# Kernel tuning notes

Measured on AMD Instinct MI355X. Metric: run time of the kernel, lower is better.

Reference implementation:

```python
import jax, jax.numpy as jnp
import numpy as np

IDENT_SIZE = 100000
E = 1024      # embedding_dim == lstm input size
H = 2048      # hidden_dim
R = 1024      # remainder_dim
RULES = 50000 # rules_size


def setup_inputs() -> dict:
    key = jax.random.key(0)
    ks = jax.random.split(key, 12)
    def w(k, shape, scale=0.02):
        return jax.random.normal(k, shape, dtype=jnp.float32) * scale
    return {
        "ident": jax.random.randint(ks[0], (1,), 0, IDENT_SIZE),
        "remainder": jax.random.normal(ks[1], (1, 1, R), dtype=jnp.float32),
        "h0": jax.random.normal(ks[2], (1, 1, H), dtype=jnp.float32),
        "c0": jax.random.normal(ks[3], (1, 1, H), dtype=jnp.float32),
        "emb": w(ks[4], (IDENT_SIZE, E)),
        "W_rin": w(ks[5], (R, E)),   # linear_remainder_in, stored [in, out]
        "b_rin": jnp.zeros((E,), jnp.float32),
        "W_ih": w(ks[6], (4 * H, E)),  # torch LSTM weight_ih_l0, gate order i,f,g,o
        "W_hh": w(ks[7], (4 * H, H)),  # torch LSTM weight_hh_l0
        "b_ih": jnp.zeros((4 * H,), jnp.float32),
        "b_hh": jnp.zeros((4 * H,), jnp.float32),
        "W_ro": w(ks[8], (H, R)),      # linear_remainder_out
        "b_ro": jnp.zeros((R,), jnp.float32),
        "W_out": w(ks[9], (H, RULES)),  # linear_out
        "b_out": jnp.zeros((RULES,), jnp.float32),
    }


def reference(ident, remainder, h0, c0, emb, W_rin, b_rin, W_ih, W_hh,
              b_ih, b_hh, W_ro, b_ro, W_out, b_out):
    # embeds = embedding(ident).view((1,-1))  -> [1, E]
    embeds = emb[ident].reshape(1, -1)
    # inputs = embeds + relu(linear_remainder_in(remainder)) -> broadcast [1,1,E]
    x = embeds + jax.nn.relu(remainder @ W_rin + b_rin)  # [1,1,E]
    # single-step LSTM (seq=1, batch=1), torch gate order i, f, g, o
    gates = x @ W_ih.T + b_ih + h0 @ W_hh.T + b_hh  # [1,1,4H]
    i, f, g, o = jnp.split(gates, 4, axis=-1)
    c = jax.nn.sigmoid(f) * c0 + jax.nn.sigmoid(i) * jnp.tanh(g)
    h = jax.nn.sigmoid(o) * jnp.tanh(c)  # lstm_out == h for seq=1
    remainder_out = jax.nn.relu(h @ W_ro + b_ro)             # [1,1,R]
    out = jax.nn.log_softmax(jax.nn.relu(h @ W_out + b_out), axis=2)  # [1,1,RULES]
    return (out, (h, c), remainder_out)
```

## Files before the change

### kernel.cpp

```cpp
#include <hip/hip_runtime.h>
#include <math.h>

#define E_DIM 1024
#define H_DIM 2048
#define R_DIM 1024
#define RULES 50000

#define OUT_H  50000
#define OUT_C  52048
#define OUT_RO 54096

#define WS_XP    0
#define WS_H     8192
#define WS_PL    10240
#define WS_LOG   810240
#define WS_BSUM  860240
#define WS_PRO   860292

__device__ __forceinline__ float sigf(float x) { return 1.f / (1.f + expf(-x)); }

__global__ __launch_bounds__(256) void k_x_partial(const float* __restrict__ rem,
    const float* __restrict__ W_rin, float* __restrict__ xp)
{
    __shared__ float rs[128];
    int ec = blockIdx.x, rc = blockIdx.y;
    if (threadIdx.x < 128) rs[threadIdx.x] = rem[rc * 128 + threadIdx.x];
    __syncthreads();
    int e = ec * 256 + threadIdx.x;
    const float* base = W_rin + (size_t)rc * 128 * E_DIM + e;
    float acc = 0.f;
#pragma unroll 8
    for (int rr = 0; rr < 128; ++rr)
        acc = fmaf(rs[rr], base[(size_t)rr * E_DIM], acc);
    xp[rc * E_DIM + e] = acc;
}

__global__ __launch_bounds__(256) void k_lstm(const float* __restrict__ xp,
    const float* __restrict__ b_rin, const float* __restrict__ emb,
    const int* __restrict__ ident,
    const float* __restrict__ h0, const float* __restrict__ c0,
    const float* __restrict__ W_ih, const float* __restrict__ W_hh,
    const float* __restrict__ b_ih, const float* __restrict__ b_hh,
    float* __restrict__ d_out, float* __restrict__ ws_h)
{
    __shared__ float xs[E_DIM];
    long long row = (long long)ident[0] * E_DIM;
#pragma unroll
    for (int e = threadIdx.x; e < E_DIM; e += 256) {
        float s = 0.f;
#pragma unroll
        for (int rc = 0; rc < 8; ++rc) s += xp[rc * E_DIM + e];
        xs[e] = emb[row + e] + fmaxf(s + b_rin[e], 0.f);
    }
    __syncthreads();

    int k = blockIdx.x;
    int w = threadIdx.x >> 6, lane = threadIdx.x & 63;
    int j = w * H_DIM + k;
    const float4* Wi = (const float4*)(W_ih + (size_t)j * E_DIM);
    const float4* Wh = (const float4*)(W_hh + (size_t)j * H_DIM);
    const float4* x4 = (const float4*)xs;
    const float4* h4 = (const float4*)h0;
    float acc = 0.f;
#pragma unroll
    for (int s = 0; s < 4; ++s) {
        int idx = s * 64 + lane;
        float4 wv = Wi[idx], xv = x4[idx];
        acc += wv.x * xv.x + wv.y * xv.y + wv.z * xv.z + wv.w * xv.w;
    }
#pragma unroll
    for (int s = 0; s < 8; ++s) {
        int idx = s * 64 + lane;
        float4 wv = Wh[idx], hv = h4[idx];
        acc += wv.x * hv.x + wv.y * hv.y + wv.z * hv.z + wv.w * hv.w;
    }
#pragma unroll
    for (int off = 32; off > 0; off >>= 1) acc += __shfl_xor(acc, off);
    __shared__ float gl[4];
    if (lane == 0) gl[w] = acc + b_ih[j] + b_hh[j];
    __syncthreads();
    if (threadIdx.x == 0) {
        float gi = gl[0], gf = gl[1], gg = gl[2], go = gl[3];
        float c = sigf(gf) * c0[k] + sigf(gi) * tanhf(gg);
        float h = sigf(go) * tanhf(c);
        d_out[OUT_H + k] = h;
        d_out[OUT_C + k] = c;
        ws_h[k] = h;
    }
}

__global__ __launch_bounds__(256) void k_big_partial(const float* __restrict__ h,
    const float* __restrict__ W_out, const float* __restrict__ W_ro,
    float* __restrict__ pl, float* __restrict__ pro)
{
    __shared__ float hs[128];
    int hc = blockIdx.y;
    if (threadIdx.x < 128) hs[threadIdx.x] = h[hc * 128 + threadIdx.x];
    __syncthreads();
    if (blockIdx.x < 49) {
        int j0 = blockIdx.x * 1024 + threadIdx.x * 4;
        if (j0 >= RULES) return;
        float4 acc = {0.f, 0.f, 0.f, 0.f};
        const float* base = W_out + (size_t)hc * 128 * RULES + j0;
#pragma unroll 8
        for (int hh = 0; hh < 128; ++hh) {
            float hv = hs[hh];
            float4 wv = *(const float4*)(base + (size_t)hh * RULES);
            acc.x = fmaf(hv, wv.x, acc.x);
            acc.y = fmaf(hv, wv.y, acc.y);
            acc.z = fmaf(hv, wv.z, acc.z);
            acc.w = fmaf(hv, wv.w, acc.w);
        }
        *(float4*)(pl + (size_t)hc * RULES + j0) = acc;
    } else {
        int j0 = threadIdx.x * 4;
        float4 acc = {0.f, 0.f, 0.f, 0.f};
        const float* base = W_ro + (size_t)hc * 128 * R_DIM + j0;
#pragma unroll 8
        for (int hh = 0; hh < 128; ++hh) {
            float hv = hs[hh];
            float4 wv = *(const float4*)(base + (size_t)hh * R_DIM);
            acc.x = fmaf(hv, wv.x, acc.x);
            acc.y = fmaf(hv, wv.y, acc.y);
            acc.z = fmaf(hv, wv.z, acc.z);
            acc.w = fmaf(hv, wv.w, acc.w);
        }
        *(float4*)(pro + hc * R_DIM + j0) = acc;
    }
}

__global__ __launch_bounds__(256) void k_final(const float* __restrict__ pl,
    const float* __restrict__ b_out, const float* __restrict__ pro,
    const float* __restrict__ b_ro, float* __restrict__ logits,
    float* __restrict__ bsum, float* __restrict__ out_ro)
{
    if (blockIdx.x < 49) {
        int j0 = blockIdx.x * 1024 + threadIdx.x * 4;
        float se = 0.f;
        if (j0 < RULES) {
            float4 s = {0.f, 0.f, 0.f, 0.f};
#pragma unroll
            for (int hc = 0; hc < 16; ++hc) {
                float4 p = *(const float4*)(pl + (size_t)hc * RULES + j0);
                s.x += p.x; s.y += p.y; s.z += p.z; s.w += p.w;
            }
            float4 b = *(const float4*)(b_out + j0);
            float4 l;
            l.x = fmaxf(s.x + b.x, 0.f);
            l.y = fmaxf(s.y + b.y, 0.f);
            l.z = fmaxf(s.z + b.z, 0.f);
            l.w = fmaxf(s.w + b.w, 0.f);
            *(float4*)(logits + j0) = l;
            se = expf(l.x) + expf(l.y) + expf(l.z) + expf(l.w);
        }
        __shared__ float red[256];
        red[threadIdx.x] = se;
        __syncthreads();
        for (int off = 128; off > 0; off >>= 1) {
            if (threadIdx.x < off) red[threadIdx.x] += red[threadIdx.x + off];
            __syncthreads();
        }
        if (threadIdx.x == 0) bsum[blockIdx.x] = red[0];
    } else {
        int j0 = threadIdx.x * 4;
        float4 s = {0.f, 0.f, 0.f, 0.f};
#pragma unroll
        for (int hc = 0; hc < 16; ++hc) {
            float4 p = *(const float4*)(pro + hc * R_DIM + j0);
            s.x += p.x; s.y += p.y; s.z += p.z; s.w += p.w;
        }
        float4 b = *(const float4*)(b_ro + j0);
        float4 o;
        o.x = fmaxf(s.x + b.x, 0.f);
        o.y = fmaxf(s.y + b.y, 0.f);
        o.z = fmaxf(s.z + b.z, 0.f);
        o.w = fmaxf(s.w + b.w, 0.f);
        *(float4*)(out_ro + j0) = o;
    }
}

__global__ __launch_bounds__(256) void k_out(const float* __restrict__ logits,
    const float* __restrict__ bsum, float* __restrict__ d_out)
{
    __shared__ float lse_s;
    if (threadIdx.x == 0) {
        float s = 0.f;
        for (int i = 0; i < 49; ++i) s += bsum[i];
        lse_s = logf(s);
    }
    __syncthreads();
    int j = blockIdx.x * 256 + threadIdx.x;
    if (j < RULES) d_out[j] = logits[j] - lse_s;
}

extern "C" void kernel_launch(void* const* d_in, const int* in_sizes, int n_in,
                              void* d_out, int out_size, void* d_ws, size_t ws_size,
                              hipStream_t stream)
{
    const int*   ident = (const int*)  d_in[0];
    const float* rem   = (const float*)d_in[1];
    const float* h0    = (const float*)d_in[2];
    const float* c0    = (const float*)d_in[3];
    const float* emb   = (const float*)d_in[4];
    const float* W_rin = (const float*)d_in[5];
    const float* b_rin = (const float*)d_in[6];
    const float* W_ih  = (const float*)d_in[7];
    const float* W_hh  = (const float*)d_in[8];
    const float* b_ih  = (const float*)d_in[9];
    const float* b_hh  = (const float*)d_in[10];
    const float* W_ro  = (const float*)d_in[11];
    const float* b_ro  = (const float*)d_in[12];
    const float* W_out = (const float*)d_in[13];
    const float* b_out = (const float*)d_in[14];
    float* out = (float*)d_out;
    float* ws  = (float*)d_ws;

    k_x_partial<<<dim3(4, 8), 256, 0, stream>>>(rem, W_rin, ws + WS_XP);
    k_lstm<<<2048, 256, 0, stream>>>(ws + WS_XP, b_rin, emb, ident,
                                     h0, c0, W_ih, W_hh, b_ih, b_hh,
                                     out, ws + WS_H);
    k_big_partial<<<dim3(50, 16), 256, 0, stream>>>(ws + WS_H, W_out, W_ro,
                                                    ws + WS_PL, ws + WS_PRO);
    k_final<<<50, 256, 0, stream>>>(ws + WS_PL, b_out, ws + WS_PRO, b_ro,
                                    ws + WS_LOG, ws + WS_BSUM, out + OUT_RO);
    k_out<<<196, 256, 0, stream>>>(ws + WS_LOG, ws + WS_BSUM, out);
}
```

Measured before the change: 123.1 us.

## Fuse final softmax kernels via atomic grid barrier, add nontemporal loads, split hidden more

Merges the reduction, logits and normalization kernels into one tail kernel. A global atomic counter lets every block wait until all 49 partial exp-sums are written, which removes one launch and the logits round-trip through workspace. Weight streams now use nontemporal loads, and the big GEMV splits the hidden dimension into 32 chunks instead of 16 for more parallelism. The cost is twice the partial-sum traffic, plus reliance on all 50 tail blocks being co-resident for the spin barrier.

```diff
diff --git a/kernel.cpp b/kernel.cpp
--- a/kernel.cpp
+++ b/kernel.cpp
@@ -12,16 +12,24 @@
 
 #define WS_XP    0
 #define WS_H     8192
-#define WS_PL    10240
-#define WS_LOG   810240
-#define WS_BSUM  860240
-#define WS_PRO   860292
+#define WS_CNT   10240
+#define WS_PL    10256
+#define WS_PRO   1610256
+#define WS_BSUM  1643024
+
+typedef float f32x4 __attribute__((ext_vector_type(4)));
+
+__device__ __forceinline__ f32x4 nt4(const float* p) {
+    return __builtin_nontemporal_load((const f32x4*)p);
+}
 
 __device__ __forceinline__ float sigf(float x) { return 1.f / (1.f + expf(-x)); }
 
 __global__ __launch_bounds__(256) void k_x_partial(const float* __restrict__ rem,
-    const float* __restrict__ W_rin, float* __restrict__ xp)
-{
+    const float* __restrict__ W_rin, float* __restrict__ xp,
+    unsigned int* __restrict__ cnt)
+{
+    if (blockIdx.x == 0 && blockIdx.y == 0 && threadIdx.x == 0) *cnt = 0u;
     __shared__ float rs[128];
     int ec = blockIdx.x, rc = blockIdx.y;
     if (threadIdx.x < 128) rs[threadIdx.x] = rem[rc * 128 + threadIdx.x];
@@ -57,21 +65,23 @@
     int k = blockIdx.x;
     int w = threadIdx.x >> 6, lane = threadIdx.x & 63;
     int j = w * H_DIM + k;
-    const float4* Wi = (const float4*)(W_ih + (size_t)j * E_DIM);
-    const float4* Wh = (const float4*)(W_hh + (size_t)j * H_DIM);
-    const float4* x4 = (const float4*)xs;
-    const float4* h4 = (const float4*)h0;
+    const float* Wi = W_ih + (size_t)j * E_DIM;
+    const float* Wh = W_hh + (size_t)j * H_DIM;
+    const f32x4* x4 = (const f32x4*)xs;
+    const f32x4* h4 = (const f32x4*)h0;
     float acc = 0.f;
 #pragma unroll
     for (int s = 0; s < 4; ++s) {
         int idx = s * 64 + lane;
-        float4 wv = Wi[idx], xv = x4[idx];
+        f32x4 wv = nt4(Wi + idx * 4);
+        f32x4 xv = x4[idx];
         acc += wv.x * xv.x + wv.y * xv.y + wv.z * xv.z + wv.w * xv.w;
     }
 #pragma unroll
     for (int s = 0; s < 8; ++s) {
         int idx = s * 64 + lane;
-        float4 wv = Wh[idx], hv = h4[idx];
+        f32x4 wv = nt4(Wh + idx * 4);
+        f32x4 hv = h4[idx];
         acc += wv.x * hv.x + wv.y * hv.y + wv.z * hv.z + wv.w * hv.w;
     }
 #pragma unroll
@@ -89,108 +99,109 @@
     }
 }
 
-__global__ __launch_bounds__(256) void k_big_partial(const float* __restrict__ h,
+__global__ __launch_bounds__(256) void k_big(const float* __restrict__ h,
     const float* __restrict__ W_out, const float* __restrict__ W_ro,
     float* __restrict__ pl, float* __restrict__ pro)
 {
-    __shared__ float hs[128];
+    __shared__ float hs[64];
     int hc = blockIdx.y;
-    if (threadIdx.x < 128) hs[threadIdx.x] = h[hc * 128 + threadIdx.x];
+    if (threadIdx.x < 64) hs[threadIdx.x] = h[hc * 64 + threadIdx.x];
     __syncthreads();
     if (blockIdx.x < 49) {
         int j0 = blockIdx.x * 1024 + threadIdx.x * 4;
         if (j0 >= RULES) return;
-        float4 acc = {0.f, 0.f, 0.f, 0.f};
-        const float* base = W_out + (size_t)hc * 128 * RULES + j0;
-#pragma unroll 8
-        for (int hh = 0; hh < 128; ++hh) {
+        f32x4 acc = {0.f, 0.f, 0.f, 0.f};
+        const float* base = W_out + (size_t)hc * 64 * RULES + j0;
+#pragma unroll 16
+        for (int hh = 0; hh < 64; ++hh) {
             float hv = hs[hh];
-            float4 wv = *(const float4*)(base + (size_t)hh * RULES);
+            f32x4 wv = nt4(base + (size_t)hh * RULES);
             acc.x = fmaf(hv, wv.x, acc.x);
             acc.y = fmaf(hv, wv.y, acc.y);
             acc.z = fmaf(hv, wv.z, acc.z);
             acc.w = fmaf(hv, wv.w, acc.w);
         }
-        *(float4*)(pl + (size_t)hc * RULES + j0) = acc;
+        *(f32x4*)(pl + (size_t)hc * RULES + j0) = acc;
     } else {
         int j0 = threadIdx.x * 4;
-        float4 acc = {0.f, 0.f, 0.f, 0.f};
-        const float* base = W_ro + (size_t)hc * 128 * R_DIM + j0;
-#pragma unroll 8
-        for (int hh = 0; hh < 128; ++hh) {
+        f32x4 acc = {0.f, 0.f, 0.f, 0.f};
+        const float* base = W_ro + (size_t)hc * 64 * R_DIM + j0;
+#pragma unroll 16
+        for (int hh = 0; hh < 64; ++hh) {
             float hv = hs[hh];
-            float4 wv = *(const float4*)(base + (size_t)hh * R_DIM);
+            f32x4 wv = nt4(base + (size_t)hh * R_DIM);
             acc.x = fmaf(hv, wv.x, acc.x);
             acc.y = fmaf(hv, wv.y, acc.y);
             acc.z = fmaf(hv, wv.z, acc.z);
             acc.w = fmaf(hv, wv.w, acc.w);
         }
-        *(float4*)(pro + hc * R_DIM + j0) = acc;
-    }
-}
-
-__global__ __launch_bounds__(256) void k_final(const float* __restrict__ pl,
+        *(f32x4*)(pro + (size_t)hc * R_DIM + j0) = acc;
+    }
+}
+
+__global__ __launch_bounds__(256) void k_tail(const float* __restrict__ pl,
     const float* __restrict__ b_out, const float* __restrict__ pro,
-    const float* __restrict__ b_ro, float* __restrict__ logits,
-    float* __restrict__ bsum, float* __restrict__ out_ro)
-{
-    if (blockIdx.x < 49) {
-        int j0 = blockIdx.x * 1024 + threadIdx.x * 4;
-        float se = 0.f;
-        if (j0 < RULES) {
-            float4 s = {0.f, 0.f, 0.f, 0.f};
-#pragma unroll
-            for (int hc = 0; hc < 16; ++hc) {
-                float4 p = *(const float4*)(pl + (size_t)hc * RULES + j0);
-                s.x += p.x; s.y += p.y; s.z += p.z; s.w += p.w;
-            }
-            float4 b = *(const float4*)(b_out + j0);
-            float4 l;
-            l.x = fmaxf(s.x + b.x, 0.f);
-            l.y = fmaxf(s.y + b.y, 0.f);
-            l.z = fmaxf(s.z + b.z, 0.f);
-            l.w = fmaxf(s.w + b.w, 0.f);
-            *(float4*)(logits + j0) = l;
-            se = expf(l.x) + expf(l.y) + expf(l.z) + expf(l.w);
-        }
-        __shared__ float red[256];
-        red[threadIdx.x] = se;
-        __syncthreads();
-        for (int off = 128; off > 0; off >>= 1) {
-            if (threadIdx.x < off) red[threadIdx.x] += red[threadIdx.x + off];
-            __syncthreads();
-        }
-        if (threadIdx.x == 0) bsum[blockIdx.x] = red[0];
-    } else {
+    const float* __restrict__ b_ro, unsigned int* __restrict__ cnt,
+    float* __restrict__ bsum, float* __restrict__ d_out)
+{
+    if (blockIdx.x == 49) {
         int j0 = threadIdx.x * 4;
-        float4 s = {0.f, 0.f, 0.f, 0.f};
-#pragma unroll
-        for (int hc = 0; hc < 16; ++hc) {
-            float4 p = *(const float4*)(pro + hc * R_DIM + j0);
+        f32x4 s = {0.f, 0.f, 0.f, 0.f};
+#pragma unroll
+        for (int hc = 0; hc < 32; ++hc) {
+            f32x4 p = *(const f32x4*)(pro + (size_t)hc * R_DIM + j0);
             s.x += p.x; s.y += p.y; s.z += p.z; s.w += p.w;
         }
-        float4 b = *(const float4*)(b_ro + j0);
-        float4 o;
+        const f32x4 b = *(const f32x4*)(b_ro + j0);
+        f32x4 o;
         o.x = fmaxf(s.x + b.x, 0.f);
         o.y = fmaxf(s.y + b.y, 0.f);
         o.z = fmaxf(s.z + b.z, 0.f);
         o.w = fmaxf(s.w + b.w, 0.f);
-        *(float4*)(out_ro + j0) = o;
-    }
-}
-
-__global__ __launch_bounds__(256) void k_out(const float* __restrict__ logits,
-    const float* __restrict__ bsum, float* __restrict__ d_out)
-{
+        *(f32x4*)(d_out + OUT_RO + j0) = o;
+        return;
+    }
+    int j0 = blockIdx.x * 1024 + threadIdx.x * 4;
+    bool valid = j0 < RULES;
+    f32x4 l = {0.f, 0.f, 0.f, 0.f};
+    float se = 0.f;
+    if (valid) {
+        f32x4 s = {0.f, 0.f, 0.f, 0.f};
+#pragma unroll
+        for (int hc = 0; hc < 32; ++hc) {
+            f32x4 p = *(const f32x4*)(pl + (size_t)hc * RULES + j0);
+            s.x += p.x; s.y += p.y; s.z += p.z; s.w += p.w;
+        }
+        const f32x4 b = *(const f32x4*)(b_out + j0);
+        l.x = fmaxf(s.x + b.x, 0.f);
+        l.y = fmaxf(s.y + b.y, 0.f);
+        l.z = fmaxf(s.z + b.z, 0.f);
+        l.w = fmaxf(s.w + b.w, 0.f);
+        se = expf(l.x) + expf(l.y) + expf(l.z) + expf(l.w);
+    }
+    __shared__ float red[256];
+    red[threadIdx.x] = se;
+    __syncthreads();
+    for (int off = 128; off > 0; off >>= 1) {
+        if (threadIdx.x < off) red[threadIdx.x] += red[threadIdx.x + off];
+        __syncthreads();
+    }
     __shared__ float lse_s;
     if (threadIdx.x == 0) {
-        float s = 0.f;
-        for (int i = 0; i < 49; ++i) s += bsum[i];
-        lse_s = logf(s);
-    }
-    __syncthreads();
-    int j = blockIdx.x * 256 + threadIdx.x;
-    if (j < RULES) d_out[j] = logits[j] - lse_s;
+        bsum[blockIdx.x] = red[0];
+        __threadfence();
+        __hip_atomic_fetch_add(cnt, 1u, __ATOMIC_RELEASE, __HIP_MEMORY_SCOPE_AGENT);
+        while (__hip_atomic_load(cnt, __ATOMIC_ACQUIRE, __HIP_MEMORY_SCOPE_AGENT) < 49u) {}
+        float ssum = 0.f;
+        for (int i = 0; i < 49; ++i) ssum += bsum[i];
+        lse_s = logf(ssum);
+    }
+    __syncthreads();
+    if (valid) {
+        f32x4 o;
+        o.x = l.x - lse_s; o.y = l.y - lse_s; o.z = l.z - lse_s; o.w = l.w - lse_s;
+        *(f32x4*)(d_out + j0) = o;
+    }
 }
 
 extern "C" void kernel_launch(void* const* d_in, const int* in_sizes, int n_in,
@@ -214,14 +225,14 @@
     const float* b_out = (const float*)d_in[14];
     float* out = (float*)d_out;
     float* ws  = (float*)d_ws;
-
-    k_x_partial<<<dim3(4, 8), 256, 0, stream>>>(rem, W_rin, ws + WS_XP);
+    unsigned int* cnt = (unsigned int*)(ws + WS_CNT);
+
+    k_x_partial<<<dim3(4, 8), 256, 0, stream>>>(rem, W_rin, ws + WS_XP, cnt);
     k_lstm<<<2048, 256, 0, stream>>>(ws + WS_XP, b_rin, emb, ident,
                                      h0, c0, W_ih, W_hh, b_ih, b_hh,
                                      out, ws + WS_H);
-    k_big_partial<<<dim3(50, 16), 256, 0, stream>>>(ws + WS_H, W_out, W_ro,
-                                                    ws + WS_PL, ws + WS_PRO);
-    k_final<<<50, 256, 0, stream>>>(ws + WS_PL, b_out, ws + WS_PRO, b_ro,
-                                    ws + WS_LOG, ws + WS_BSUM, out + OUT_RO);
-    k_out<<<196, 256, 0, stream>>>(ws + WS_LOG, ws + WS_BSUM, out);
-}
+    k_big<<<dim3(50, 32), 256, 0, stream>>>(ws + WS_H, W_out, W_ro,
+                                            ws + WS_PL, ws + WS_PRO);
+    k_tail<<<50, 256, 0, stream>>>(ws + WS_PL, b_out, ws + WS_PRO, b_ro,
+                                   cnt, ws + WS_BSUM, out);
+}
```

New measurement: 110.9 us. 1.11x faster.
